# Kernel optimization log

Measured on AMD Instinct MI355X. Metric: run time of the kernel, lower is better.

## Reference

```python
import jax, jax.numpy as jnp
import numpy as np

B, S, D = 4, 4096, 2048
DECAY_BIAS_INIT = -4.0
W_SCALE = 0.02


def setup_inputs() -> dict:
    key = jax.random.key(0)
    ks = jax.random.split(key, 6)
    return {
        "x": jax.random.normal(ks[0], (B, S, D), dtype=jnp.float32),
        "W_in": jax.random.normal(ks[1], (D, D), dtype=jnp.float32) * W_SCALE,
        "b_in": jnp.zeros((D,), jnp.float32),
        "W_decay": jax.random.normal(ks[2], (D, D), dtype=jnp.float32) * W_SCALE,
        "b_decay": jnp.zeros((D,), jnp.float32),
        "W_gate": jax.random.normal(ks[3], (D, D), dtype=jnp.float32) * W_SCALE,
        "b_gate": jnp.zeros((D,), jnp.float32),
        "W_out": jax.random.normal(ks[4], (D, D), dtype=jnp.float32) * W_SCALE,
        "b_out": jnp.zeros((D,), jnp.float32),
        "decay_bias": jnp.full((D,), DECAY_BIAS_INIT, jnp.float32),
    }


def reference(x, W_in, b_in, W_decay, b_decay, W_gate, b_gate, W_out, b_out, decay_bias):
    # Projections (weights stored as [in, out]; torch Linear applies x @ W.T, here W is pre-transposed)
    inp = jax.nn.silu(jnp.einsum("bsd,de->bse", x, W_in) + b_in).astype(jnp.float32)
    decay = jax.nn.sigmoid(jnp.einsum("bsd,de->bse", x, W_decay) + b_decay + decay_bias)
    gate = jax.nn.sigmoid(jnp.einsum("bsd,de->bse", x, W_gate) + b_gate)

    # Gated linear recurrence: s_t = d_t * s_{t-1} + (1 - d_t) * i_t
    def step(state, di):
        d, i = di
        state = d * state + (1.0 - d) * i
        return state, state

    init = jnp.zeros((x.shape[0], x.shape[2]), jnp.float32)
    _, states = jax.lax.scan(
        step, init, (jnp.swapaxes(decay, 0, 1), jnp.swapaxes(inp, 0, 1))
    )  # states: [S, B, D]
    y = gate * jnp.swapaxes(states, 0, 1)  # [B, S, D]
    y = y.astype(x.dtype)
    return jnp.einsum("bsd,de->bse", y, W_out) + b_out
```

## Files before the change

kernel.cpp:

```cpp
#include <hip/hip_runtime.h>

typedef unsigned short u16;
typedef __attribute__((ext_vector_type(4))) float f4;
typedef __attribute__((ext_vector_type(8))) short s8v;
typedef __attribute__((ext_vector_type(8))) unsigned short u16x8;
typedef __attribute__((ext_vector_type(4))) unsigned short u16x4;

#define B_   4
#define S_   4096
#define D_   2048
#define M_   (B_ * S_)
#define K_   D_
#define N3_  (3 * D_)
#define CCH  128
#define LCH  32
#define NTK  32

__device__ __forceinline__ u16 f2bf(float f) {
  unsigned u = __float_as_uint(f);
  u += 0x7FFF + ((u >> 16) & 1);
  return (u16)(u >> 16);
}
__device__ __forceinline__ float bf2f(u16 h) {
  return __uint_as_float(((unsigned)h) << 16);
}
__device__ __forceinline__ float sigm(float z) {
  return 1.0f / (1.0f + __expf(-z));
}

__global__ void k_cvt(const float* __restrict__ src, u16* __restrict__ dst, int n4) {
  int i = blockIdx.x * 256 + threadIdx.x;
  if (i >= n4) return;
  f4 v = *(const f4*)(src + (size_t)i * 4);
  u16x4 o;
  o[0] = f2bf(v[0]); o[1] = f2bf(v[1]); o[2] = f2bf(v[2]); o[3] = f2bf(v[3]);
  *(u16x4*)(dst + (size_t)i * 4) = o;
}

__global__ void k_tcvt(const float* __restrict__ src, u16* __restrict__ dst) {
  __shared__ float tile[32][33];
  int tx = threadIdx.x & 31, ty = threadIdx.x >> 5;
  int c0 = blockIdx.x * 32, r0 = blockIdx.y * 32;
#pragma unroll
  for (int j = 0; j < 32; j += 8)
    tile[ty + j][tx] = src[(size_t)(r0 + ty + j) * 2048 + c0 + tx];
  __syncthreads();
#pragma unroll
  for (int j = 0; j < 32; j += 8)
    dst[(size_t)(c0 + ty + j) * 2048 + r0 + tx] = f2bf(tile[tx][ty + j]);
}

__global__ void __launch_bounds__(512, 2)
k_gemm256(const u16* __restrict__ A, const u16* __restrict__ BT, int N, int mode,
          u16* __restrict__ o_inp, u16* __restrict__ o_dec, u16* __restrict__ o_gate,
          const float* __restrict__ b_in, const float* __restrict__ b_dec,
          const float* __restrict__ b_gate, const float* __restrict__ dbias,
          float* __restrict__ o_f, const float* __restrict__ b_out) {
  extern __shared__ u16 smem[];
  u16* const Asb[2] = { smem,         smem + 16384 };
  u16* const Bsb[2] = { smem + 32768, smem + 49152 };

  const int bid = blockIdx.x;
  const int xcd = bid & 7, j = bid >> 3;
  const int nsb = j >> 6;
  const int rj = j & 63;
  const int mm = rj >> 3, nn = rj & 7;
  const int tile_m = ((xcd << 3) + mm) << 8;
  const int tile_n = ((nsb << 3) + nn) << 8;

  const int tid = threadIdx.x;
  const int wave = tid >> 6, lane = tid & 63;
  const int wm = (wave >> 2) << 7;
  const int wn = (wave & 3) << 6;
  const int l15 = lane & 15, lhi = lane >> 4;
  const int srow = tid >> 3, sslot = tid & 7;

  f4 acc[8][4];
#pragma unroll
  for (int m = 0; m < 8; ++m)
#pragma unroll
    for (int n = 0; n < 4; ++n)
#pragma unroll
      for (int r = 0; r < 4; ++r) acc[m][n][r] = 0.0f;

  s8v afr2[2][2][2];
  s8v bfr[2][4];

  const int swz = l15 & 7;
  const u16* ap[2][2];
  const u16* bp[2][2];
#pragma unroll
  for (int b = 0; b < 2; ++b)
#pragma unroll
    for (int kk = 0; kk < 2; ++kk) {
      const int so = ((((kk << 2) + lhi) ^ swz) << 3);
      ap[b][kk] = Asb[b] + ((wm + l15) << 6) + so;
      bp[b][kk] = Bsb[b] + ((wn + l15) << 6) + so;
    }
  const int gl = srow * K_ + ((sslot ^ (srow & 7)) << 3);

  auto STAGE = [&](const u16* __restrict__ G, int grow0, u16* L, int c, int k0) {
    const u16* src = G + (size_t)(grow0 + (c << 6)) * K_ + k0;
    __builtin_amdgcn_global_load_lds(
        (const __attribute__((address_space(1))) unsigned int*)(src + gl),
        (__attribute__((address_space(3))) unsigned int*)(L + (((c << 6) + (wave << 3)) << 6)),
        16, 0, 0);
  };

#pragma unroll
  for (int c = 0; c < 4; ++c) STAGE(A, tile_m, Asb[0], c, 0);
#pragma unroll
  for (int c = 0; c < 4; ++c) STAGE(BT, tile_n, Bsb[0], c, 0);
#pragma unroll
  for (int c = 0; c < 4; ++c) STAGE(BT, tile_n, Bsb[1], c, 64);
  STAGE(A, tile_m, Asb[1], 0, 64);
  STAGE(A, tile_m, Asb[1], 2, 64);
  asm volatile("s_waitcnt vmcnt(6)" ::: "memory");
  __builtin_amdgcn_s_barrier();

#pragma unroll
  for (int kk = 0; kk < 2; ++kk)
#pragma unroll
    for (int mi = 0; mi < 2; ++mi)
      afr2[0][mi][kk] = *(const s8v*)(ap[0][kk] + (mi << 10));
#pragma unroll
  for (int kk = 0; kk < 2; ++kk)
#pragma unroll
    for (int n = 0; n < 4; ++n)
      bfr[kk][n] = *(const s8v*)(bp[0][kk] + (n << 10));

#pragma unroll 1
  for (int it = 0; it < NTK / 2; ++it) {
    const int t0 = it << 1;
#pragma unroll
    for (int p = 0; p < 8; ++p) {
      const int toff[8] = {1, 2, 2, 2, 2, 3, 3, 3};
      const int sopA[8] = {1, 0, 0, 1, 1, 0, 0, 1};
      const int sc0[8]  = {1, 0, 2, 0, 1, 0, 2, 0};
      const int sc1f[8] = {3, 1, 3, 2, 3, 1, 3, 2};
      const int q = p & 3;

      {
        const int st = (t0 + toff[p]) & (NTK - 1);
        const int k0s = st << 6;
        u16* const Ad = Asb[st & 1];
        u16* const Bd = Bsb[st & 1];
        if (sopA[p]) { STAGE(A, tile_m, Ad, sc0[p], k0s); STAGE(A, tile_m, Ad, sc1f[p], k0s); }
        else         { STAGE(BT, tile_n, Bd, sc0[p], k0s); STAGE(BT, tile_n, Bd, sc1f[p], k0s); }
      }
      if (q == 3) {
        asm volatile("s_waitcnt vmcnt(6)" ::: "memory");
        __builtin_amdgcn_sched_barrier(0);
      }
      __builtin_amdgcn_s_barrier();

      {
        const int pn = p + 1;
        const int qn = pn & 3, bn = (pn >> 2) & 1, as = pn & 1;
#pragma unroll
        for (int kk = 0; kk < 2; ++kk)
#pragma unroll
          for (int mi = 0; mi < 2; ++mi)
            afr2[as][mi][kk] = *(const s8v*)(ap[bn][kk] + (((qn << 1) + mi) << 10));
      }

      __builtin_amdgcn_s_setprio(1);
#pragma unroll
      for (int kk = 0; kk < 2; ++kk)
#pragma unroll
        for (int mi = 0; mi < 2; ++mi)
#pragma unroll
          for (int n = 0; n < 4; ++n)
            acc[q * 2 + mi][n] =
                __builtin_amdgcn_mfma_f32_16x16x32_bf16(afr2[p & 1][mi][kk], bfr[kk][n],
                                                        acc[q * 2 + mi][n], 0, 0, 0);
      __builtin_amdgcn_s_setprio(0);

      if (q == 3) {
        const int bn = ((p + 1) >> 2) & 1;
#pragma unroll
        for (int kk = 0; kk < 2; ++kk)
#pragma unroll
          for (int n = 0; n < 4; ++n)
            bfr[kk][n] = *(const s8v*)(bp[bn][kk] + (n << 10));
      }
      __builtin_amdgcn_s_barrier();
    }
  }

  asm volatile("s_waitcnt vmcnt(0)" ::: "memory");
  __builtin_amdgcn_s_barrier();

  if (mode == 0) {
    const int selb = tile_n >> 11;
    const int dbase = tile_n & 2047;
    float bias[4];
#pragma unroll
    for (int n = 0; n < 4; ++n) {
      int d = dbase + wn + (n << 4) + l15;
      bias[n] = (selb == 0) ? b_in[d] : (selb == 1) ? (b_dec[d] + dbias[d]) : b_gate[d];
    }
#pragma unroll
    for (int m = 0; m < 8; ++m)
#pragma unroll
      for (int n = 0; n < 4; ++n)
#pragma unroll
        for (int r = 0; r < 4; ++r) {
          int lrow = wm + (m << 4) + (lhi << 2) + r;
          int lcol = wn + (n << 4) + l15;
          float z = acc[m][n][r] + bias[n];
          float v = (selb == 0) ? z * sigm(z) : sigm(z);
          smem[(lrow << 8) + (((lcol >> 3) ^ (lrow & 7)) << 3) + (lcol & 7)] = f2bf(v);
        }
    __builtin_amdgcn_s_barrier();
    u16* const dst = (selb == 0) ? o_inp : (selb == 1) ? o_dec : o_gate;
    const int rr = tid >> 5, sl = tid & 31;
#pragma unroll
    for (int pass = 0; pass < 16; ++pass) {
      int row = (pass << 4) + rr;
      u16x8 v = *(const u16x8*)(smem + (row << 8) + ((sl ^ (row & 7)) << 3));
      *(u16x8*)(dst + (size_t)(tile_m + row) * D_ + dbase + (sl << 3)) = v;
    }
  } else {
    float* const Tf = (float*)smem;
    f4 bo = *(const f4*)(b_out + tile_n + (lane << 2));
#pragma unroll
    for (int sw = 0; sw < 2; ++sw) {
      if (sw) __builtin_amdgcn_s_barrier();
      if ((wm >> 7) == sw) {
#pragma unroll
        for (int m = 0; m < 8; ++m)
#pragma unroll
          for (int n = 0; n < 4; ++n)
#pragma unroll
            for (int r = 0; r < 4; ++r) {
              int lrow = (m << 4) + (lhi << 2) + r;
              int lcol = wn + (n << 4) + l15;
              Tf[(lrow << 8) + (((lcol >> 2) ^ (lrow & 7)) << 2) + (lcol & 3)] = acc[m][n][r];
            }
      }
      __builtin_amdgcn_s_barrier();
#pragma unroll
      for (int pass = 0; pass < 16; ++pass) {
        int lrow = (pass << 3) + wave;
        f4 v = *(const f4*)(Tf + (lrow << 8) + ((lane ^ (lrow & 7)) << 2));
        v[0] += bo[0]; v[1] += bo[1]; v[2] += bo[2]; v[3] += bo[3];
        *(f4*)(o_f + (size_t)(tile_m + (sw << 7) + lrow) * D_ + tile_n + (lane << 2)) = v;
      }
    }
  }
}

__global__ void k_scan1(const u16* __restrict__ dec, const u16* __restrict__ inp,
                        float* __restrict__ chA, float* __restrict__ chB) {
  int b = blockIdx.x / CCH, c = blockIdx.x % CCH;
  int d0 = threadIdx.x * 8;
  const u16* dp = dec + ((size_t)b * S_ + c * LCH) * D_ + d0;
  const u16* ip = inp + ((size_t)b * S_ + c * LCH) * D_ + d0;
  float Aa[8], st[8];
#pragma unroll
  for (int i = 0; i < 8; ++i) { Aa[i] = 1.0f; st[i] = 0.0f; }
#pragma unroll 4
  for (int j = 0; j < LCH; ++j) {
    u16x8 dv = *(const u16x8*)(dp + (size_t)j * D_);
    u16x8 iv = *(const u16x8*)(ip + (size_t)j * D_);
#pragma unroll
    for (int i = 0; i < 8; ++i) {
      float dd = bf2f(dv[i]), ii = bf2f(iv[i]);
      Aa[i] *= dd;
      st[i] = dd * st[i] + (1.0f - dd) * ii;
    }
  }
  size_t o = ((size_t)b * CCH + c) * D_ + d0;
#pragma unroll
  for (int i = 0; i < 8; ++i) { chA[o + i] = Aa[i]; chB[o + i] = st[i]; }
}

__global__ void k_scan2(const float* __restrict__ chA, const float* __restrict__ chB,
                        float* __restrict__ ini) {
  int b = blockIdx.x >> 3;
  int d = ((blockIdx.x & 7) << 8) + threadIdx.x;
  float st = 0.0f;
  for (int c = 0; c < CCH; ++c) {
    size_t o = ((size_t)b * CCH + c) * D_ + d;
    ini[o] = st;
    st = chA[o] * st + chB[o];
  }
}

__global__ void k_scan3(const u16* __restrict__ dec, const u16* __restrict__ inp,
                        const u16* __restrict__ gat, const float* __restrict__ ini,
                        u16* __restrict__ y) {
  int b = blockIdx.x / CCH, c = blockIdx.x % CCH;
  int d0 = threadIdx.x * 8;
  size_t ib = ((size_t)b * CCH + c) * D_ + d0;
  float st[8];
#pragma unroll
  for (int i = 0; i < 8; ++i) st[i] = ini[ib + i];
  size_t base = ((size_t)b * S_ + c * LCH) * D_ + d0;
#pragma unroll 4
  for (int j = 0; j < LCH; ++j) {
    size_t o = base + (size_t)j * D_;
    u16x8 dv = *(const u16x8*)(dec + o);
    u16x8 iv = *(const u16x8*)(inp + o);
    u16x8 gv = *(const u16x8*)(gat + o);
    u16x8 yv;
#pragma unroll
    for (int i = 0; i < 8; ++i) {
      float dd = bf2f(dv[i]), ii = bf2f(iv[i]);
      st[i] = dd * st[i] + (1.0f - dd) * ii;
      yv[i] = f2bf(bf2f(gv[i]) * st[i]);
    }
    *(u16x8*)(y + o) = yv;
  }
}

extern "C" void kernel_launch(void* const* d_in, const int* in_sizes, int n_in,
                              void* d_out, int out_size, void* d_ws, size_t ws_size,
                              hipStream_t stream) {
  (void)in_sizes; (void)n_in; (void)out_size; (void)ws_size;
  const float* x      = (const float*)d_in[0];
  const float* W_in   = (const float*)d_in[1];
  const float* b_in   = (const float*)d_in[2];
  const float* W_dec  = (const float*)d_in[3];
  const float* b_dec  = (const float*)d_in[4];
  const float* W_gate = (const float*)d_in[5];
  const float* b_gate = (const float*)d_in[6];
  const float* W_out  = (const float*)d_in[7];
  const float* b_out  = (const float*)d_in[8];
  const float* dbias  = (const float*)d_in[9];
  float* out = (float*)d_out;

  char* ws = (char*)d_ws;
  u16*   xb  = (u16*)(ws);
  u16*   w3t = (u16*)(ws + 67108864ull);
  u16*   wot = (u16*)(ws + 92274688ull);
  u16*   inp = (u16*)(ws + 100663296ull);
  u16*   dec = (u16*)(ws + 167772160ull);
  u16*   gat = (u16*)(ws + 234881024ull);
  float* chA = (float*)(ws + 301989888ull);
  float* chB = (float*)(ws + 306184192ull);
  float* ini = (float*)(ws + 310378496ull);
  u16*   y   = xb;

  hipFuncSetAttribute((const void*)k_gemm256,
                      hipFuncAttributeMaxDynamicSharedMemorySize, 131072);

  k_cvt<<<32768, 256, 0, stream>>>(x, xb, 8388608);
  k_tcvt<<<dim3(64, 64), 256, 0, stream>>>(W_in,   w3t);
  k_tcvt<<<dim3(64, 64), 256, 0, stream>>>(W_dec,  w3t + 2048 * 2048);
  k_tcvt<<<dim3(64, 64), 256, 0, stream>>>(W_gate, w3t + 2 * 2048 * 2048);
  k_tcvt<<<dim3(64, 64), 256, 0, stream>>>(W_out,  wot);

  k_gemm256<<<(M_ / 256) * (N3_ / 256), 512, 131072, stream>>>(
      xb, w3t, N3_, 0, inp, dec, gat, b_in, b_dec, b_gate, dbias, nullptr, nullptr);

  k_scan1<<<B_ * CCH, 256, 0, stream>>>(dec, inp, chA, chB);
  k_scan2<<<32, 256, 0, stream>>>(chA, chB, ini);
  k_scan3<<<B_ * CCH, 256, 0, stream>>>(dec, inp, gat, ini, y);

  k_gemm256<<<(M_ / 256) * (D_ / 256), 512, 131072, stream>>>(
      y, wot, D_, 1, nullptr, nullptr, nullptr, nullptr, nullptr, nullptr, nullptr,
      out, b_out);
}
```

Measured before the change: 651.9 us.

## Switch GEMM to 32x32x16 MFMA tiles, drop a barrier, fuse weight transposes

Rewrites the GEMM inner loop to use 32x32x16 bf16 MFMA instructions instead of 16x16x32. Fragment loads, the accumulator layout and both epilogues are adjusted to match. The larger instruction tile needs fewer LDS fragment reads per FLOP and fewer MFMA issues. The trailing per-phase barrier in the main loop is removed, which cuts synchronisation but risks an LDS write/read race with the next staged load. The four weight-transpose launches are merged into one 3D-grid launch.

New measurement: 697.1 us. +6.9%, slower.

```diff
diff --git a/kernel.cpp b/kernel.cpp
--- a/kernel.cpp
+++ b/kernel.cpp
@@ -2,6 +2,7 @@
 
 typedef unsigned short u16;
 typedef __attribute__((ext_vector_type(4))) float f4;
+typedef __attribute__((ext_vector_type(16))) float f16v;
 typedef __attribute__((ext_vector_type(8))) short s8v;
 typedef __attribute__((ext_vector_type(8))) unsigned short u16x8;
 typedef __attribute__((ext_vector_type(4))) unsigned short u16x4;
@@ -37,8 +38,13 @@
   *(u16x4*)(dst + (size_t)i * 4) = o;
 }
 
-__global__ void k_tcvt(const float* __restrict__ src, u16* __restrict__ dst) {
+__global__ void k_tcvt4(const float* __restrict__ W_in, const float* __restrict__ W_dec,
+                        const float* __restrict__ W_gate, const float* __restrict__ W_out,
+                        u16* __restrict__ w3t, u16* __restrict__ wot) {
   __shared__ float tile[32][33];
+  const float* src = (blockIdx.z == 0) ? W_in : (blockIdx.z == 1) ? W_dec
+                    : (blockIdx.z == 2) ? W_gate : W_out;
+  u16* dst = (blockIdx.z < 3) ? (w3t + (size_t)blockIdx.z * 2048 * 2048) : wot;
   int tx = threadIdx.x & 31, ty = threadIdx.x >> 5;
   int c0 = blockIdx.x * 32, r0 = blockIdx.y * 32;
 #pragma unroll
@@ -61,9 +67,9 @@
   u16* const Bsb[2] = { smem + 32768, smem + 49152 };
 
   const int bid = blockIdx.x;
-  const int xcd = bid & 7, j = bid >> 3;
-  const int nsb = j >> 6;
-  const int rj = j & 63;
+  const int xcd = bid & 7, j0 = bid >> 3;
+  const int nsb = j0 >> 6;
+  const int rj = j0 & 63;
   const int mm = rj >> 3, nn = rj & 7;
   const int tile_m = ((xcd << 3) + mm) << 8;
   const int tile_n = ((nsb << 3) + nn) << 8;
@@ -72,33 +78,34 @@
   const int wave = tid >> 6, lane = tid & 63;
   const int wm = (wave >> 2) << 7;
   const int wn = (wave & 3) << 6;
-  const int l15 = lane & 15, lhi = lane >> 4;
+  const int l31 = lane & 31, lk = lane >> 5;
+  const int lhi = lane >> 4;
   const int srow = tid >> 3, sslot = tid & 7;
 
-  f4 acc[8][4];
-#pragma unroll
-  for (int m = 0; m < 8; ++m)
-#pragma unroll
-    for (int n = 0; n < 4; ++n)
-#pragma unroll
-      for (int r = 0; r < 4; ++r) acc[m][n][r] = 0.0f;
-
-  s8v afr2[2][2][2];
+  f16v acc[4][2];
+#pragma unroll
+  for (int m = 0; m < 4; ++m)
+#pragma unroll
+    for (int n = 0; n < 2; ++n)
+#pragma unroll
+      for (int r = 0; r < 16; ++r) acc[m][n][r] = 0.0f;
+
+  s8v afr2[2][4];
   s8v bfr[2][4];
 
-  const int swz = l15 & 7;
-  const u16* ap[2][2];
-  const u16* bp[2][2];
-#pragma unroll
-  for (int b = 0; b < 2; ++b)
-#pragma unroll
-    for (int kk = 0; kk < 2; ++kk) {
-      const int so = ((((kk << 2) + lhi) ^ swz) << 3);
-      ap[b][kk] = Asb[b] + ((wm + l15) << 6) + so;
-      bp[b][kk] = Bsb[b] + ((wn + l15) << 6) + so;
-    }
+  const int rsw = l31 & 7;
+  auto ARD = [&](u16* Ab, int q, int jj) -> s8v {
+    int row = wm + (q << 5) + l31;
+    int s = (jj << 1) + lk;
+    return *(const s8v*)(Ab + (row << 6) + ((s ^ rsw) << 3));
+  };
+  auto BRD = [&](u16* Bb, int nf, int jj) -> s8v {
+    int row = wn + (nf << 5) + l31;
+    int s = (jj << 1) + lk;
+    return *(const s8v*)(Bb + (row << 6) + ((s ^ rsw) << 3));
+  };
+
   const int gl = srow * K_ + ((sslot ^ (srow & 7)) << 3);
-
   auto STAGE = [&](const u16* __restrict__ G, int grow0, u16* L, int c, int k0) {
     const u16* src = G + (size_t)(grow0 + (c << 6)) * K_ + k0;
     __builtin_amdgcn_global_load_lds(
@@ -119,15 +126,11 @@
   __builtin_amdgcn_s_barrier();
 
 #pragma unroll
-  for (int kk = 0; kk < 2; ++kk)
-#pragma unroll
-    for (int mi = 0; mi < 2; ++mi)
-      afr2[0][mi][kk] = *(const s8v*)(ap[0][kk] + (mi << 10));
-#pragma unroll
-  for (int kk = 0; kk < 2; ++kk)
-#pragma unroll
-    for (int n = 0; n < 4; ++n)
-      bfr[kk][n] = *(const s8v*)(bp[0][kk] + (n << 10));
+  for (int jj = 0; jj < 4; ++jj) afr2[0][jj] = ARD(Asb[0], 0, jj);
+#pragma unroll
+  for (int nf = 0; nf < 2; ++nf)
+#pragma unroll
+    for (int jj = 0; jj < 4; ++jj) bfr[nf][jj] = BRD(Bsb[0], nf, jj);
 
 #pragma unroll 1
   for (int it = 0; it < NTK / 2; ++it) {
@@ -158,33 +161,25 @@
         const int pn = p + 1;
         const int qn = pn & 3, bn = (pn >> 2) & 1, as = pn & 1;
 #pragma unroll
-        for (int kk = 0; kk < 2; ++kk)
-#pragma unroll
-          for (int mi = 0; mi < 2; ++mi)
-            afr2[as][mi][kk] = *(const s8v*)(ap[bn][kk] + (((qn << 1) + mi) << 10));
+        for (int jj = 0; jj < 4; ++jj) afr2[as][jj] = ARD(Asb[bn], qn, jj);
       }
 
       __builtin_amdgcn_s_setprio(1);
 #pragma unroll
-      for (int kk = 0; kk < 2; ++kk)
-#pragma unroll
-        for (int mi = 0; mi < 2; ++mi)
-#pragma unroll
-          for (int n = 0; n < 4; ++n)
-            acc[q * 2 + mi][n] =
-                __builtin_amdgcn_mfma_f32_16x16x32_bf16(afr2[p & 1][mi][kk], bfr[kk][n],
-                                                        acc[q * 2 + mi][n], 0, 0, 0);
+      for (int jj = 0; jj < 4; ++jj)
+#pragma unroll
+        for (int nf = 0; nf < 2; ++nf)
+          acc[q][nf] = __builtin_amdgcn_mfma_f32_32x32x16_bf16(
+              afr2[p & 1][jj], bfr[nf][jj], acc[q][nf], 0, 0, 0);
       __builtin_amdgcn_s_setprio(0);
 
       if (q == 3) {
         const int bn = ((p + 1) >> 2) & 1;
 #pragma unroll
-        for (int kk = 0; kk < 2; ++kk)
-#pragma unroll
-          for (int n = 0; n < 4; ++n)
-            bfr[kk][n] = *(const s8v*)(bp[bn][kk] + (n << 10));
-      }
-      __builtin_amdgcn_s_barrier();
+        for (int nf = 0; nf < 2; ++nf)
+#pragma unroll
+          for (int jj = 0; jj < 4; ++jj) bfr[nf][jj] = BRD(Bsb[bn], nf, jj);
+      }
     }
   }
 
@@ -194,23 +189,23 @@
   if (mode == 0) {
     const int selb = tile_n >> 11;
     const int dbase = tile_n & 2047;
-    float bias[4];
-#pragma unroll
-    for (int n = 0; n < 4; ++n) {
-      int d = dbase + wn + (n << 4) + l15;
-      bias[n] = (selb == 0) ? b_in[d] : (selb == 1) ? (b_dec[d] + dbias[d]) : b_gate[d];
-    }
-#pragma unroll
-    for (int m = 0; m < 8; ++m)
-#pragma unroll
-      for (int n = 0; n < 4; ++n)
-#pragma unroll
-        for (int r = 0; r < 4; ++r) {
-          int lrow = wm + (m << 4) + (lhi << 2) + r;
-          int lcol = wn + (n << 4) + l15;
-          float z = acc[m][n][r] + bias[n];
-          float v = (selb == 0) ? z * sigm(z) : sigm(z);
-          smem[(lrow << 8) + (((lcol >> 3) ^ (lrow & 7)) << 3) + (lcol & 7)] = f2bf(v);
+    float bias[2];
+#pragma unroll
+    for (int nf = 0; nf < 2; ++nf) {
+      int d = dbase + wn + (nf << 5) + l31;
+      bias[nf] = (selb == 0) ? b_in[d] : (selb == 1) ? (b_dec[d] + dbias[d]) : b_gate[d];
+    }
+#pragma unroll
+    for (int mf = 0; mf < 4; ++mf)
+#pragma unroll
+      for (int nf = 0; nf < 2; ++nf)
+#pragma unroll
+        for (int v = 0; v < 16; ++v) {
+          int lrow = wm + (mf << 5) + (v & 3) + ((v >> 2) << 3) + (lk << 2);
+          int lcol = wn + (nf << 5) + l31;
+          float z = acc[mf][nf][v] + bias[nf];
+          float val = (selb == 0) ? z * sigm(z) : sigm(z);
+          smem[(lrow << 8) + (((lcol >> 3) ^ (lrow & 7)) << 3) + (lcol & 7)] = f2bf(val);
         }
     __builtin_amdgcn_s_barrier();
     u16* const dst = (selb == 0) ? o_inp : (selb == 1) ? o_dec : o_gate;
@@ -229,14 +224,14 @@
       if (sw) __builtin_amdgcn_s_barrier();
       if ((wm >> 7) == sw) {
 #pragma unroll
-        for (int m = 0; m < 8; ++m)
-#pragma unroll
-          for (int n = 0; n < 4; ++n)
-#pragma unroll
-            for (int r = 0; r < 4; ++r) {
-              int lrow = (m << 4) + (lhi << 2) + r;
-              int lcol = wn + (n << 4) + l15;
-              Tf[(lrow << 8) + (((lcol >> 2) ^ (lrow & 7)) << 2) + (lcol & 3)] = acc[m][n][r];
+        for (int mf = 0; mf < 4; ++mf)
+#pragma unroll
+          for (int nf = 0; nf < 2; ++nf)
+#pragma unroll
+            for (int v = 0; v < 16; ++v) {
+              int lrow = (mf << 5) + (v & 3) + ((v >> 2) << 3) + (lk << 2);
+              int lcol = wn + (nf << 5) + l31;
+              Tf[(lrow << 8) + (((lcol >> 2) ^ (lrow & 7)) << 2) + (lcol & 3)] = acc[mf][nf][v];
             }
       }
       __builtin_amdgcn_s_barrier();
@@ -249,6 +244,7 @@
       }
     }
   }
+  (void)lhi;
 }
 
 __global__ void k_scan1(const u16* __restrict__ dec, const u16* __restrict__ inp,
@@ -347,10 +343,7 @@
                       hipFuncAttributeMaxDynamicSharedMemorySize, 131072);
 
   k_cvt<<<32768, 256, 0, stream>>>(x, xb, 8388608);
-  k_tcvt<<<dim3(64, 64), 256, 0, stream>>>(W_in,   w3t);
-  k_tcvt<<<dim3(64, 64), 256, 0, stream>>>(W_dec,  w3t + 2048 * 2048);
-  k_tcvt<<<dim3(64, 64), 256, 0, stream>>>(W_gate, w3t + 2 * 2048 * 2048);
-  k_tcvt<<<dim3(64, 64), 256, 0, stream>>>(W_out,  wot);
+  k_tcvt4<<<dim3(64, 64, 4), 256, 0, stream>>>(W_in, W_dec, W_gate, W_out, w3t, wot);
 
   k_gemm256<<<(M_ / 256) * (N3_ / 256), 512, 131072, stream>>>(
       xb, w3t, N3_, 0, inp, dec, gat, b_in, b_dec, b_gate, dbias, nullptr, nullptr);
```
